# Performance work log

Hardware: AMD Instinct MI355X
Metric: run time of the kernel (lower is better)

Reference implementation:

```python
import jax, jax.numpy as jnp
import numpy as np

N0 = 50000
N1 = 50000
E = 500000
IN_DIM = 128
OUT_DIM = 128
H = 8
DK = OUT_DIM // H  # 16
SQRT_DK = float(np.sqrt(DK))
NUM_TYPES = 2
NUM_REL = 3
# relations: (src_type, dst_type, e_id)
RELATIONS = [(0, 1, 0), (1, 0, 1), (0, 0, 2)]


def setup_inputs() -> dict:
    key = jax.random.key(0)
    ks = jax.random.split(key, 24)
    d = {}
    d["h0"] = jax.random.normal(ks[0], (N0, IN_DIM), dtype=jnp.float32)
    d["h1"] = jax.random.normal(ks[1], (N1, IN_DIM), dtype=jnp.float32)
    d["src0"] = jax.random.randint(ks[2], (E,), 0, N0)
    d["dst0"] = jax.random.randint(ks[3], (E,), 0, N1)
    d["src1"] = jax.random.randint(ks[4], (E,), 0, N1)
    d["dst1"] = jax.random.randint(ks[5], (E,), 0, N0)
    d["src2"] = jax.random.randint(ks[6], (E,), 0, N0)
    d["dst2"] = jax.random.randint(ks[7], (E,), 0, N0)
    w_scale = 1.0 / np.sqrt(IN_DIM)
    # per-node-type stacked linear weights (k, q, v, a), torch Linear convention: y = x @ W.T + b
    d["Wk"] = jax.random.normal(ks[8], (NUM_TYPES, OUT_DIM, IN_DIM), dtype=jnp.float32) * w_scale
    d["bk"] = jnp.zeros((NUM_TYPES, OUT_DIM), dtype=jnp.float32)
    d["Wq"] = jax.random.normal(ks[9], (NUM_TYPES, OUT_DIM, IN_DIM), dtype=jnp.float32) * w_scale
    d["bq"] = jnp.zeros((NUM_TYPES, OUT_DIM), dtype=jnp.float32)
    d["Wv"] = jax.random.normal(ks[10], (NUM_TYPES, OUT_DIM, IN_DIM), dtype=jnp.float32) * w_scale
    d["bv"] = jnp.zeros((NUM_TYPES, OUT_DIM), dtype=jnp.float32)
    d["Wa"] = jax.random.normal(ks[11], (NUM_TYPES, OUT_DIM, OUT_DIM), dtype=jnp.float32) * w_scale
    d["ba"] = jnp.zeros((NUM_TYPES, OUT_DIM), dtype=jnp.float32)
    xavier = float(np.sqrt(6.0 / (DK + DK)))
    d["rel_att"] = jax.random.uniform(ks[12], (NUM_REL, H, DK, DK), dtype=jnp.float32, minval=-xavier, maxval=xavier)
    d["rel_msg"] = jax.random.uniform(ks[13], (NUM_REL, H, DK, DK), dtype=jnp.float32, minval=-xavier, maxval=xavier)
    d["rel_pri"] = jnp.ones((NUM_REL, H), dtype=jnp.float32)
    d["skip"] = jnp.ones((NUM_TYPES,), dtype=jnp.float32)
    return d


def _lin(x, W, b):
    return x @ W.T + b


def reference(h0, h1, src0, dst0, src1, dst1, src2, dst2,
              Wk, bk, Wq, bq, Wv, bv, Wa, ba,
              rel_att, rel_msg, rel_pri, skip):
    h = [h0, h1]
    edges = [(src0, dst0), (src1, dst1), (src2, dst2)]
    # per-type projections, reshaped to (N, H, DK)
    k = [_lin(h[t], Wk[t], bk[t]).reshape(-1, H, DK) for t in range(NUM_TYPES)]
    q = [_lin(h[t], Wq[t], bq[t]).reshape(-1, H, DK) for t in range(NUM_TYPES)]
    v = [_lin(h[t], Wv[t], bv[t]).reshape(-1, H, DK) for t in range(NUM_TYPES)]

    agg = [[] for _ in range(NUM_TYPES)]
    for (s, dt, e), (src, dst) in zip(RELATIONS, edges):
        # relation-specific transforms of source k and v
        kr = jnp.einsum('nhi,hij->nhj', k[s], rel_att[e])
        vr = jnp.einsum('nhi,hij->nhj', v[s], rel_msg[e])
        # per-edge dot-product score (E, H)
        score = (q[dt][dst] * kr[src]).sum(-1) * rel_pri[e] / SQRT_DK
        n_dst = h[dt].shape[0]
        # edge softmax normalized by dst (stable)
        m = jax.ops.segment_max(score, dst, num_segments=n_dst)
        ex = jnp.exp(score - m[dst])
        den = jax.ops.segment_sum(ex, dst, num_segments=n_dst)
        attn = ex / den[dst]  # (E, H)
        # weighted message scatter-sum -> (n_dst, H, DK)
        msg = vr[src] * attn[:, :, None]
        agg[dt].append(jax.ops.segment_sum(msg, dst, num_segments=n_dst))

    new_h = []
    for t in range(NUM_TYPES):
        # cross_reducer='mean' over relations targeting this node type
        tmean = sum(agg[t]) / float(len(agg[t]))
        tflat = tmean.reshape(-1, OUT_DIM)
        trans = _lin(tflat, Wa[t], ba[t])  # dropout = identity (eval)
        alpha = jax.nn.sigmoid(skip[t])
        new_h.append(trans * alpha + h[t] * (1.0 - alpha))
    return tuple(new_h)
```

## Files before the change

### kernel.cpp

```cpp
#include <hip/hip_runtime.h>

typedef __attribute__((ext_vector_type(8))) short bf16x8;
typedef __attribute__((ext_vector_type(4))) float f32x4;

#define NB 196
#define CHK 2048
#define CAPB 4096

__device__ __forceinline__ float bflo(unsigned u) { return __uint_as_float(u << 16); }
__device__ __forceinline__ float bfhi(unsigned u) { return __uint_as_float(u & 0xFFFF0000u); }
__device__ __forceinline__ unsigned f2bf(float f) {
  unsigned u = __float_as_uint(f);
  u = (u + 0x7FFFu + ((u >> 16) & 1u)) >> 16;
  return u;
}

__global__ void cvt2_kernel(const float* __restrict__ a, unsigned short* __restrict__ oa,
                            const float* __restrict__ b, unsigned short* __restrict__ ob,
                            int n8) {
  int i = blockIdx.x * 256 + threadIdx.x;
  if (i >= n8) return;
  const float* in = blockIdx.y ? b : a;
  unsigned short* out = blockIdx.y ? ob : oa;
  const float4* p = (const float4*)(in + (size_t)i * 8);
  float4 x = p[0], y = p[1];
  uint4 v;
  v.x = f2bf(x.x) | (f2bf(x.y) << 16);
  v.y = f2bf(x.z) | (f2bf(x.w) << 16);
  v.z = f2bf(y.x) | (f2bf(y.y) << 16);
  v.w = f2bf(y.z) | (f2bf(y.w) << 16);
  *(uint4*)(out + (size_t)i * 8) = v;
}

__global__ void compose_w_kernel(const float* __restrict__ Wk, const float* __restrict__ bk,
                                 const float* __restrict__ Wv, const float* __restrict__ bv,
                                 const float* __restrict__ rel_att, const float* __restrict__ rel_msg,
                                 const float* __restrict__ rel_pri,
                                 unsigned short* __restrict__ Wkr, float* __restrict__ bkr,
                                 unsigned short* __restrict__ Wvr, float* __restrict__ bvr) {
  int e = blockIdx.x;
  int o = blockIdx.y;
  int z = blockIdx.z;
  int c = threadIdx.x;
  int hd = o >> 4, j = o & 15;
  const int se[3] = {0, 1, 0};
  int s = se[e];
  const float* W = z ? Wv : Wk;
  const float* b = z ? bv : bk;
  const float* R = z ? rel_msg : rel_att;
  float scale = z ? 1.0f : (rel_pri[e * 8 + hd] * 0.25f);
  float acc = 0.0f, bacc = 0.0f;
#pragma unroll
  for (int i = 0; i < 16; ++i) {
    float r = R[((e * 8 + hd) * 16 + i) * 16 + j];
    acc += W[(s * 128 + hd * 16 + i) * 128 + c] * r;
    bacc += b[s * 128 + hd * 16 + i] * r;
  }
  unsigned short* Wo = z ? Wvr : Wkr;
  float* bo = z ? bvr : bkr;
  Wo[((size_t)e * 128 + o) * 128 + c] = (unsigned short)f2bf(acc * scale);
  if (c == 0) bo[e * 128 + o] = bacc * scale;
}

struct ProjFP {
  const float* A[2];
  int M[2];
  int nj[2];
  const unsigned short* W[10];
  const float* b[10];
  unsigned short* out[10];
  int ostr[10];
};

__global__ __launch_bounds__(256) void proj_gemm_fused(ProjFP P) {
  __shared__ short As[128 * 128];
  __shared__ short Bs[128 * 128];
  int type = blockIdx.y;
  const float* __restrict__ A = P.A[type];
  int M = P.M[type];
  int nj = P.nj[type];
  int base = type * 5;
  int row0 = blockIdx.x * 128;
  if (row0 >= M) return;
  int t = threadIdx.x;
  bool full = (row0 + 128 <= M);
#pragma unroll
  for (int it = 0; it < 8; ++it) {
    int o = (it * 256 + t) * 8;
    int row = o >> 7, col = o & 127;
    int gr = row0 + row;
    uint4 av = make_uint4(0, 0, 0, 0);
    if (full || gr < M) {
      float4 x = *(const float4*)(A + (size_t)gr * 128 + col);
      float4 y = *(const float4*)(A + (size_t)gr * 128 + col + 4);
      av.x = f2bf(x.x) | (f2bf(x.y) << 16);
      av.y = f2bf(x.z) | (f2bf(x.w) << 16);
      av.z = f2bf(y.x) | (f2bf(y.y) << 16);
      av.w = f2bf(y.z) | (f2bf(y.w) << 16);
    }
    int sw = o ^ ((row & 7) << 3);
    *(uint4*)(&As[sw]) = av;
  }
  {
    const unsigned short* W0 = P.W[base];
#pragma unroll
    for (int it = 0; it < 8; ++it) {
      int o = (it * 256 + t) * 8;
      int row = o >> 7;
      int sw = o ^ ((row & 7) << 3);
      *(uint4*)(&Bs[sw]) = *(const uint4*)(W0 + o);
    }
  }
  __syncthreads();
  int wid = t >> 6, l = t & 63;
  int wr = wid >> 1, wc = wid & 1;
  int lr = l & 15, kb = l >> 4;
  for (int j = 0;; ++j) {
    f32x4 acc[4][4] = {};
#pragma unroll
    for (int ks = 0; ks < 4; ++ks) {
      bf16x8 af[4], bfr[4];
#pragma unroll
      for (int m = 0; m < 4; ++m) {
        int row = wr * 64 + m * 16 + lr;
        int h = (row * 128 + kb * 8 + ks * 32) ^ ((row & 7) << 3);
        af[m] = *(bf16x8*)(&As[h]);
      }
#pragma unroll
      for (int n = 0; n < 4; ++n) {
        int row = wc * 64 + n * 16 + lr;
        int h = (row * 128 + kb * 8 + ks * 32) ^ ((row & 7) << 3);
        bfr[n] = *(bf16x8*)(&Bs[h]);
      }
#pragma unroll
      for (int m = 0; m < 4; ++m)
#pragma unroll
        for (int n = 0; n < 4; ++n)
          acc[m][n] = __builtin_amdgcn_mfma_f32_16x16x32_bf16(af[m], bfr[n], acc[m][n], 0, 0, 0);
    }
    const float* bias = P.b[base + j];
    unsigned short* out = P.out[base + j];
    int ostr = P.ostr[base + j];
    int rb = row0 + wr * 64 + (l >> 4) * 4;
#pragma unroll
    for (int m = 0; m < 4; ++m)
#pragma unroll
      for (int jr = 0; jr < 4; ++jr) {
        int grow = rb + m * 16 + jr;
        if (grow < M) {
#pragma unroll
          for (int n = 0; n < 4; ++n) {
            int col = wc * 64 + n * 16 + lr;
            out[(size_t)grow * ostr + col] = (unsigned short)f2bf(acc[m][n][jr] + bias[col]);
          }
        }
      }
    if (j + 1 >= nj) break;
    __syncthreads();
    {
      const unsigned short* Wj = P.W[base + j + 1];
#pragma unroll
      for (int it = 0; it < 8; ++it) {
        int o = (it * 256 + t) * 8;
        int row = o >> 7;
        int sw = o ^ ((row & 7) << 3);
        *(uint4*)(&Bs[sw]) = *(const uint4*)(Wj + o);
      }
    }
    __syncthreads();
  }
}

__global__ __launch_bounds__(256) void final_gemm_mfma(
    float* __restrict__ dout, const unsigned short* __restrict__ Tb0,
    const unsigned short* __restrict__ Tb1, const unsigned short* __restrict__ Wab,
    const float* __restrict__ ba, const float* __restrict__ h0, const float* __restrict__ h1,
    const float* __restrict__ skip, int N0, int N1) {
  __shared__ short As[128 * 128];
  __shared__ short Bs[128 * 128];
  int type = blockIdx.y;
  int M = type ? N1 : N0;
  const unsigned short* T = type ? Tb1 : Tb0;
  const unsigned short* W = Wab + (size_t)type * 16384;
  const float* bias = ba + type * 128;
  const float* h = type ? h1 : h0;
  float* O = dout + (type ? (size_t)N0 * 128 : 0);
  int row0 = blockIdx.x * 128;
  if (row0 >= M) return;
  int t = threadIdx.x;
  bool full = (row0 + 128 <= M);
#pragma unroll
  for (int it = 0; it < 8; ++it) {
    int o = (it * 256 + t) * 8;
    int row = o >> 7;
    int gr = row0 + row;
    uint4 av = make_uint4(0, 0, 0, 0);
    if (full || gr < M) av = *(const uint4*)(T + (size_t)gr * 128 + (o & 127));
    int sw = o ^ ((row & 7) << 3);
    *(uint4*)(&As[sw]) = av;
    uint4 wv = *(const uint4*)(W + o);
    *(uint4*)(&Bs[sw]) = wv;
  }
  __syncthreads();
  int wid = t >> 6, l = t & 63;
  int wr = wid >> 1, wc = wid & 1;
  int lr = l & 15, kb = l >> 4;
  f32x4 acc[4][4] = {};
#pragma unroll
  for (int ks = 0; ks < 4; ++ks) {
    bf16x8 af[4], bfr[4];
#pragma unroll
    for (int m = 0; m < 4; ++m) {
      int row = wr * 64 + m * 16 + lr;
      int h2 = (row * 128 + kb * 8 + ks * 32) ^ ((row & 7) << 3);
      af[m] = *(bf16x8*)(&As[h2]);
    }
#pragma unroll
    for (int n = 0; n < 4; ++n) {
      int row = wc * 64 + n * 16 + lr;
      int h2 = (row * 128 + kb * 8 + ks * 32) ^ ((row & 7) << 3);
      bfr[n] = *(bf16x8*)(&Bs[h2]);
    }
#pragma unroll
    for (int m = 0; m < 4; ++m)
#pragma unroll
      for (int n = 0; n < 4; ++n)
        acc[m][n] = __builtin_amdgcn_mfma_f32_16x16x32_bf16(af[m], bfr[n], acc[m][n], 0, 0, 0);
  }
  float alpha = 1.0f / (1.0f + __expf(-skip[type]));
  float beta = 1.0f - alpha;
  int rb = row0 + wr * 64 + (l >> 4) * 4;
#pragma unroll
  for (int m = 0; m < 4; ++m)
#pragma unroll
    for (int jr = 0; jr < 4; ++jr) {
      int grow = rb + m * 16 + jr;
      if (grow < M) {
#pragma unroll
        for (int n = 0; n < 4; ++n) {
          int col = wc * 64 + n * 16 + lr;
          float vout = alpha * (acc[m][n][jr] + bias[col]) + beta * h[(size_t)grow * 128 + col];
          O[(size_t)grow * 128 + col] = vout;
        }
      }
    }
}


__global__ __launch_bounds__(256) void bhist_kernel(const int* __restrict__ d0,
                                                    const int* __restrict__ d1,
                                                    const int* __restrict__ d2,
                                                    int* __restrict__ bh, int E) {
  __shared__ int lh[NB];
  int r = blockIdx.y;
  const int* dst = r == 0 ? d0 : (r == 1 ? d1 : d2);
  int t = threadIdx.x;
  int lo = blockIdx.x * CHK;
  int hi = lo + CHK < E ? lo + CHK : E;
  for (int j = t; j < NB; j += 256) lh[j] = 0;
  __syncthreads();
  for (int i = lo + t; i < hi; i += 256) atomicAdd(&lh[dst[i] >> 8], 1);
  __syncthreads();
  for (int j = t; j < NB; j += 256) {
    int v = lh[j];
    if (v) atomicAdd(&bh[r * NB + j], v);
  }
}

__global__ void bscan_kernel(const int* __restrict__ bh, int* __restrict__ bbase, int E) {
  __shared__ int sdm[256];
  int r = blockIdx.x;
  int t = threadIdx.x;
  int v = (t < NB) ? bh[r * NB + t] : 0;
  sdm[t] = v;
  __syncthreads();
  for (int off = 1; off < 256; off <<= 1) {
    int u = (t >= off) ? sdm[t - off] : 0;
    __syncthreads();
    sdm[t] += u;
    __syncthreads();
  }
  if (t < NB) bbase[r * (NB + 1) + t] = sdm[t] - v;
  if (t == 0) bbase[r * (NB + 1) + NB] = E;
}

__global__ __launch_bounds__(256) void bin_kernel(
    const int* __restrict__ s0, const int* __restrict__ d0, const int* __restrict__ s1,
    const int* __restrict__ d1, const int* __restrict__ s2, const int* __restrict__ d2,
    const int* __restrict__ bbase, int* __restrict__ bcur, unsigned* __restrict__ bo0,
    unsigned* __restrict__ bo1, unsigned* __restrict__ bo2, int E) {
  __shared__ unsigned st[CHK];
  __shared__ int ga[CHK];
  __shared__ int hist[NB];
  __shared__ int scn[256];
  __shared__ int gb[NB];
  int r = blockIdx.y;
  const int* src = r == 0 ? s0 : (r == 1 ? s1 : s2);
  const int* dst = r == 0 ? d0 : (r == 1 ? d1 : d2);
  unsigned* bo = r == 0 ? bo0 : (r == 1 ? bo1 : bo2);
  const int* bb = bbase + r * (NB + 1);
  int t = threadIdx.x;
  int lo = blockIdx.x * CHK;
  int hi = lo + CHK < E ? lo + CHK : E;
  int nloc = hi - lo;
  if (nloc <= 0) return;
  for (int j = t; j < NB; j += 256) hist[j] = 0;
  __syncthreads();
  int myb[CHK / 256], myr[CHK / 256];
  unsigned mye[CHK / 256];
#pragma unroll
  for (int k = 0; k < CHK / 256; ++k) {
    int i = lo + k * 256 + t;
    myb[k] = -1;
    if (i < hi) {
      int d = dst[i];
      int b = d >> 8;
      mye[k] = (unsigned)src[i] | ((unsigned)d << 16);
      myb[k] = b;
      myr[k] = atomicAdd(&hist[b], 1);
    }
  }
  __syncthreads();
  int v = (t < NB) ? hist[t] : 0;
  scn[t] = v;
  __syncthreads();
  for (int off = 1; off < 256; off <<= 1) {
    int u = (t >= off) ? scn[t - off] : 0;
    __syncthreads();
    scn[t] += u;
    __syncthreads();
  }
  int excl = scn[t] - v;
  __syncthreads();
  scn[t] = excl;
  if (t < NB && v > 0) gb[t] = atomicAdd(&bcur[r * NB + t], v);
  __syncthreads();
#pragma unroll
  for (int k = 0; k < CHK / 256; ++k) {
    if (myb[k] >= 0) {
      int slot = scn[myb[k]] + myr[k];
      st[slot] = mye[k];
      ga[slot] = bb[myb[k]] + gb[myb[k]] + myr[k];
    }
  }
  __syncthreads();
  for (int j = t; j < nloc; j += 256) bo[ga[j]] = st[j];
}

__global__ __launch_bounds__(256) void bsort_kernel(
    const unsigned* __restrict__ bo0, const unsigned* __restrict__ bo1,
    const unsigned* __restrict__ bo2, const int* __restrict__ bbase, int* __restrict__ rp0,
    int* __restrict__ rp1, int* __restrict__ rp2, unsigned* __restrict__ sp0,
    unsigned* __restrict__ sp1, unsigned* __restrict__ sp2, int nd0, int nd1, int nd2, int E) {
  __shared__ unsigned ed[CAPB];
  __shared__ unsigned srt[CAPB];
  __shared__ unsigned short rank[CAPB];
  __shared__ int hist[256];
  __shared__ int scn[256];
  int r = blockIdx.y, b = blockIdx.x;
  const unsigned* bo = r == 0 ? bo0 : (r == 1 ? bo1 : bo2);
  int* rp = r == 0 ? rp0 : (r == 1 ? rp1 : rp2);
  unsigned* sp = r == 0 ? sp0 : (r == 1 ? sp1 : sp2);
  int nd = r == 0 ? nd0 : (r == 1 ? nd1 : nd2);
  const int* bb = bbase + r * (NB + 1);
  int base = bb[b], endb = bb[b + 1];
  int cnt = endb - base;
  if (cnt > CAPB) cnt = CAPB;
  int nlo = b << 8;
  int nn = nd - nlo;
  if (nn > 256) nn = 256;
  int t = threadIdx.x;
  hist[t] = 0;
  for (int j = t; j < cnt; j += 256) ed[j] = bo[base + j];
  __syncthreads();
  for (int j = t; j < cnt; j += 256) {
    int node = (ed[j] >> 16) & 255;
    rank[j] = (unsigned short)atomicAdd(&hist[node], 1);
  }
  __syncthreads();
  int v = hist[t];
  scn[t] = v;
  __syncthreads();
  for (int off = 1; off < 256; off <<= 1) {
    int u = (t >= off) ? scn[t - off] : 0;
    __syncthreads();
    scn[t] += u;
    __syncthreads();
  }
  int excl = scn[t] - v;
  __syncthreads();
  scn[t] = excl;
  __syncthreads();
  if (t < nn) rp[nlo + t] = base + excl;
  if (b == 0 && t == 0) rp[nd] = E;
  for (int j = t; j < cnt; j += 256) {
    int node = (ed[j] >> 16) & 255;
    srt[scn[node] + rank[j]] = ed[j];
  }
  __syncthreads();
  for (int j = t; j < cnt; j += 256) sp[base + j] = srt[j];
}

struct ScP {
  const unsigned* sp[3];
  const unsigned* kv[3];
  const unsigned* qb[3];
  unsigned short* eb[3];
  int E;
};

__global__ __launch_bounds__(256) void score_kernel(ScP P) {
  int r = blockIdx.y;
  const unsigned* __restrict__ sp = P.sp[r];
  const unsigned* __restrict__ kv = P.kv[r];
  const unsigned* __restrict__ qb = P.qb[r];
  unsigned short* __restrict__ eb = P.eb[r];
  int t = threadIdx.x;
  int p = blockIdx.x * 32 + (t >> 3);
  if (p >= P.E) return;
  int h = t & 7;
  unsigned pk = sp[p];
  unsigned s = pk & 0xFFFFu;
  unsigned d = pk >> 16;
  const uint4* kr = (const uint4*)((const char*)kv + ((size_t)s << 9) + h * 32);
  const uint4* qr = (const uint4*)((const char*)qb + ((size_t)d << 8) + h * 32);
  uint4 k1 = kr[0], k2 = kr[1];
  uint4 q1 = qr[0], q2 = qr[1];
  float sc = 0.f;
#pragma unroll
  for (int c = 0; c < 4; ++c) {
    unsigned ku = ((const unsigned*)&k1)[c], qu = ((const unsigned*)&q1)[c];
    sc = fmaf(bflo(ku), bflo(qu), sc);
    sc = fmaf(bfhi(ku), bfhi(qu), sc);
  }
#pragma unroll
  for (int c = 0; c < 4; ++c) {
    unsigned ku = ((const unsigned*)&k2)[c], qu = ((const unsigned*)&q2)[c];
    sc = fmaf(bflo(ku), bflo(qu), sc);
    sc = fmaf(bfhi(ku), bfhi(qu), sc);
  }
  eb[(size_t)p * 8 + h] = (unsigned short)f2bf(__expf(sc));
}

struct AgP {
  const unsigned *sp0, *sp1, *sp2;
  const unsigned short *eb0, *eb1, *eb2;
  const unsigned *kv0, *kv1, *kv2;
  const int *rp0, *rp1, *rp2;
  unsigned *Tb0, *Tb1;
  int N0, N1;
};

__device__ __forceinline__ void loadV(const char* __restrict__ kvl,
                                      const unsigned* __restrict__ sp, int p, int lastp,
                                      int half, uint2 vb[4]) {
  int idx = p + (threadIdx.x & 7);
  idx = idx > lastp ? lastp : idx;
  unsigned sv = sp[idx];
#pragma unroll
  for (int g = 0; g < 4; ++g) {
    unsigned plo = __builtin_amdgcn_readlane(sv, g);
    unsigned phi = __builtin_amdgcn_readlane(sv, g + 4);
    unsigned pk = half ? phi : plo;
    vb[g] = *(const uint2*)(kvl + ((size_t)(pk & 0xFFFFu) << 9));
  }
}

__device__ __forceinline__ void computeV(const unsigned short* __restrict__ eb, int p, int end,
                                         int lastp, int half, int h, const uint2 vb[4],
                                         float& a0, float& a1, float& a2, float& a3,
                                         float& den) {
#pragma unroll
  for (int g = 0; g < 4; ++g) {
    int pj = p + (half << 2) + g;
    int pj2 = pj > lastp ? lastp : pj;
    float e = __uint_as_float((unsigned)eb[(size_t)pj2 * 8 + h] << 16);
    e *= (pj < end) ? 1.f : 0.f;
    den += e;
    a0 = fmaf(e, bflo(vb[g].x), a0);
    a1 = fmaf(e, bfhi(vb[g].x), a1);
    a2 = fmaf(e, bflo(vb[g].y), a2);
    a3 = fmaf(e, bfhi(vb[g].y), a3);
  }
}

__device__ __forceinline__ void agg_rel(const unsigned* __restrict__ sp,
                                        const unsigned short* __restrict__ eb,
                                        const unsigned* __restrict__ kv,
                                        const int* __restrict__ rp, int node, int ll, int half,
                                        float& r0, float& r1, float& r2, float& r3) {
  int beg = __builtin_amdgcn_readfirstlane(rp[node]);
  int end = __builtin_amdgcn_readfirstlane(rp[node + 1]);
  if (end <= beg) return;
  int lastp = end - 1;
  int h = ll >> 2;
  const char* kvl = (const char*)kv + 256 + ll * 8;
  float a0 = 0.f, a1 = 0.f, a2 = 0.f, a3 = 0.f, den = 0.f;
  uint2 va[4], vb[4];
  int p = beg;
  loadV(kvl, sp, p, lastp, half, va);
  for (;;) {
    if (p + 8 < end) loadV(kvl, sp, p + 8, lastp, half, vb);
    computeV(eb, p, end, lastp, half, h, va, a0, a1, a2, a3, den);
    p += 8;
    if (p >= end) break;
    if (p + 8 < end) loadV(kvl, sp, p + 8, lastp, half, va);
    computeV(eb, p, end, lastp, half, h, vb, a0, a1, a2, a3, den);
    p += 8;
    if (p >= end) break;
  }
  den += __shfl_xor(den, 32);
  a0 += __shfl_xor(a0, 32);
  a1 += __shfl_xor(a1, 32);
  a2 += __shfl_xor(a2, 32);
  a3 += __shfl_xor(a3, 32);
  float inv = 1.0f / den;
  r0 = fmaf(a0, inv, r0);
  r1 = fmaf(a1, inv, r1);
  r2 = fmaf(a2, inv, r2);
  r3 = fmaf(a3, inv, r3);
}

__global__ __launch_bounds__(256) void agg2_kernel(AgP P) {
  int gw = (blockIdx.x * 256 + threadIdx.x) >> 6;
  int l = threadIdx.x & 63;
  int ll = l & 31, half = l >> 5;
  if (gw < P.N0) {
    float r0 = 0.f, r1 = 0.f, r2 = 0.f, r3 = 0.f;
    agg_rel(P.sp1, P.eb1, P.kv1, P.rp1, gw, ll, half, r0, r1, r2, r3);
    agg_rel(P.sp2, P.eb2, P.kv2, P.rp2, gw, ll, half, r0, r1, r2, r3);
    if (half == 0) {
      uint2 o;
      o.x = f2bf(r0 * 0.5f) | (f2bf(r1 * 0.5f) << 16);
      o.y = f2bf(r2 * 0.5f) | (f2bf(r3 * 0.5f) << 16);
      *(uint2*)(P.Tb0 + (size_t)gw * 64 + 2 * ll) = o;
    }
  } else if (gw < P.N0 + P.N1) {
    int n = gw - P.N0;
    float r0 = 0.f, r1 = 0.f, r2 = 0.f, r3 = 0.f;
    agg_rel(P.sp0, P.eb0, P.kv0, P.rp0, n, ll, half, r0, r1, r2, r3);
    if (half == 0) {
      uint2 o;
      o.x = f2bf(r0) | (f2bf(r1) << 16);
      o.y = f2bf(r2) | (f2bf(r3) << 16);
      *(uint2*)(P.Tb1 + (size_t)n * 64 + 2 * ll) = o;
    }
  }
}

extern "C" void kernel_launch(void* const* d_in, const int* in_sizes, int n_in,
                              void* d_out, int out_size, void* d_ws, size_t ws_size,
                              hipStream_t stream) {
  const float* h0 = (const float*)d_in[0];
  const float* h1 = (const float*)d_in[1];
  const int* srcs[3] = {(const int*)d_in[2], (const int*)d_in[4], (const int*)d_in[6]};
  const int* dsts[3] = {(const int*)d_in[3], (const int*)d_in[5], (const int*)d_in[7]};
  const float* Wk = (const float*)d_in[8];
  const float* bk = (const float*)d_in[9];
  const float* Wq = (const float*)d_in[10];
  const float* bq = (const float*)d_in[11];
  const float* Wv = (const float*)d_in[12];
  const float* bv = (const float*)d_in[13];
  const float* Wa = (const float*)d_in[14];
  const float* ba = (const float*)d_in[15];
  const float* rel_att = (const float*)d_in[16];
  const float* rel_msg = (const float*)d_in[17];
  const float* rel_pri = (const float*)d_in[18];
  const float* skip = (const float*)d_in[19];

  int N0 = in_sizes[0] / 128;
  int N1 = in_sizes[1] / 128;
  int E = in_sizes[2];
  int nsrc[3] = {N0, N1, N0};
  int ndst[3] = {N1, N0, N0};
  int maxN = N0 > N1 ? N0 : N1;

  char* base = (char*)d_ws;
  size_t off = 0;
  auto alloc = [&](size_t bytes) -> void* {
    void* p = base + off;
    off += (bytes + 255) & ~(size_t)255;
    return p;
  };

  unsigned short* qb0 = (unsigned short*)alloc((size_t)N0 * 128 * 2);
  unsigned short* qb1 = (unsigned short*)alloc((size_t)N1 * 128 * 2);
  unsigned short* kvb[3];
  for (int r = 0; r < 3; ++r) kvb[r] = (unsigned short*)alloc((size_t)nsrc[r] * 256 * 2);
  unsigned short* Tb0 = (unsigned short*)alloc((size_t)N0 * 128 * 2);
  unsigned short* Tb1 = (unsigned short*)alloc((size_t)N1 * 128 * 2);
  unsigned short* Wkrb = (unsigned short*)alloc((size_t)3 * 16384 * 2);
  unsigned short* Wvrb = (unsigned short*)alloc((size_t)3 * 16384 * 2);
  unsigned short* Wqb = (unsigned short*)alloc((size_t)2 * 16384 * 2);
  unsigned short* Wab = (unsigned short*)alloc((size_t)2 * 16384 * 2);
  float* bkr = (float*)alloc(3 * 128 * 4);
  float* bvr = (float*)alloc(3 * 128 * 4);
  int* rp[3];
  unsigned* spk[3];
  unsigned short* eb[3];
  unsigned* bo[3];
  for (int r = 0; r < 3; ++r) {
    rp[r] = (int*)alloc((size_t)(ndst[r] + 1) * 4);
    spk[r] = (unsigned*)alloc((size_t)(E + 8) * 4);
    eb[r] = (unsigned short*)alloc((size_t)E * 8 * 2);
    bo[r] = (unsigned*)alloc((size_t)(E + 8) * 4);
  }
  int* bcnt = (int*)alloc((size_t)2 * 3 * NB * 4);
  int* bhist = bcnt;
  int* bcur = bcnt + 3 * NB;
  int* bbase = (int*)alloc((size_t)3 * (NB + 1) * 4);
  (void)ws_size;

  compose_w_kernel<<<dim3(3, 128, 2), 128, 0, stream>>>(Wk, bk, Wv, bv, rel_att, rel_msg,
                                                        rel_pri, Wkrb, bkr, Wvrb, bvr);
  cvt2_kernel<<<dim3(16, 2), 256, 0, stream>>>(Wq, Wqb, Wa, Wab, 4096);

  ProjFP pf;
  pf.A[0] = h0; pf.A[1] = h1;
  pf.M[0] = N0; pf.M[1] = N1;
  pf.nj[0] = 5; pf.nj[1] = 3;
  pf.W[0] = Wqb;            pf.b[0] = bq;        pf.out[0] = qb0;          pf.ostr[0] = 128;
  pf.W[1] = Wkrb;           pf.b[1] = bkr;       pf.out[1] = kvb[0];       pf.ostr[1] = 256;
  pf.W[2] = Wkrb + 32768;   pf.b[2] = bkr + 256; pf.out[2] = kvb[2];       pf.ostr[2] = 256;
  pf.W[3] = Wvrb;           pf.b[3] = bvr;       pf.out[3] = kvb[0] + 128; pf.ostr[3] = 256;
  pf.W[4] = Wvrb + 32768;   pf.b[4] = bvr + 256; pf.out[4] = kvb[2] + 128; pf.ostr[4] = 256;
  pf.W[5] = Wqb + 16384;    pf.b[5] = bq + 128;  pf.out[5] = qb1;          pf.ostr[5] = 128;
  pf.W[6] = Wkrb + 16384;   pf.b[6] = bkr + 128; pf.out[6] = kvb[1];       pf.ostr[6] = 256;
  pf.W[7] = Wvrb + 16384;   pf.b[7] = bvr + 128; pf.out[7] = kvb[1] + 128; pf.ostr[7] = 256;
  pf.W[8] = Wqb; pf.b[8] = bq; pf.out[8] = qb0; pf.ostr[8] = 128;
  pf.W[9] = Wqb; pf.b[9] = bq; pf.out[9] = qb0; pf.ostr[9] = 128;
  proj_gemm_fused<<<dim3((maxN + 127) / 128, 2), 256, 0, stream>>>(pf);

  hipMemsetAsync(bcnt, 0, (size_t)2 * 3 * NB * 4, stream);
  bhist_kernel<<<dim3((E + CHK - 1) / CHK, 3), 256, 0, stream>>>(dsts[0], dsts[1], dsts[2],
                                                                 bhist, E);
  bscan_kernel<<<3, 256, 0, stream>>>(bhist, bbase, E);
  bin_kernel<<<dim3((E + CHK - 1) / CHK, 3), 256, 0, stream>>>(
      srcs[0], dsts[0], srcs[1], dsts[1], srcs[2], dsts[2], bbase, bcur, bo[0], bo[1], bo[2], E);
  bsort_kernel<<<dim3(NB, 3), 256, 0, stream>>>(
      bo[0], bo[1], bo[2], bbase, rp[0], rp[1], rp[2], spk[0], spk[1], spk[2], ndst[0],
      ndst[1], ndst[2], E);

  ScP sp;
  for (int r = 0; r < 3; ++r) {
    sp.sp[r] = spk[r];
    sp.kv[r] = (const unsigned*)kvb[r];
    sp.eb[r] = eb[r];
  }
  sp.qb[0] = (const unsigned*)qb1;
  sp.qb[1] = (const unsigned*)qb0;
  sp.qb[2] = (const unsigned*)qb0;
  sp.E = E;
  score_kernel<<<dim3((E + 31) / 32, 3), 256, 0, stream>>>(sp);

  AgP ap;
  ap.sp0 = spk[0]; ap.sp1 = spk[1]; ap.sp2 = spk[2];
  ap.eb0 = eb[0]; ap.eb1 = eb[1]; ap.eb2 = eb[2];
  ap.kv0 = (const unsigned*)kvb[0]; ap.kv1 = (const unsigned*)kvb[1];
  ap.kv2 = (const unsigned*)kvb[2];
  ap.rp0 = rp[0]; ap.rp1 = rp[1]; ap.rp2 = rp[2];
  ap.Tb0 = (unsigned*)Tb0; ap.Tb1 = (unsigned*)Tb1;
  ap.N0 = N0; ap.N1 = N1;
  int totw = N0 + N1;
  agg2_kernel<<<(totw + 3) / 4, 256, 0, stream>>>(ap);

  final_gemm_mfma<<<dim3((maxN + 127) / 128, 2), 256, 0, stream>>>(
      (float*)d_out, Tb0, Tb1, Wab, ba, h0, h1, skip, N0, N1);
}
```

Measured before the change: 250.0 us.

## Pad per-node edge segments to multiples of eight with head-major score layout

The bucket sort now pads each destination node's edge list to a multiple of 8 with sentinel entries and writes into fixed-stride per-bucket regions, storing separate start/end offsets per node. Scores are stored head-major within each 8-edge group, so the aggregation loop fetches all four exp weights for a lane with one 8-byte load instead of four clamped scalar loads with bounds masking. This removes the tail clamping and masking work in the aggregation inner loop. In exchange, padding adds extra gathered edges and sentinel clamping, and the score grid is oversized with early-exit blocks.

```diff
diff --git a/kernel.cpp b/kernel.cpp
--- a/kernel.cpp
+++ b/kernel.cpp
@@ -6,6 +6,7 @@
 #define NB 196
 #define CHK 2048
 #define CAPB 4096
+#define PSTRIDE 6144
 
 __device__ __forceinline__ float bflo(unsigned u) { return __uint_as_float(u << 16); }
 __device__ __forceinline__ float bfhi(unsigned u) { return __uint_as_float(u & 0xFFFF0000u); }
@@ -349,17 +350,19 @@
 
 __global__ __launch_bounds__(256) void bsort_kernel(
     const unsigned* __restrict__ bo0, const unsigned* __restrict__ bo1,
-    const unsigned* __restrict__ bo2, const int* __restrict__ bbase, int* __restrict__ rp0,
-    int* __restrict__ rp1, int* __restrict__ rp2, unsigned* __restrict__ sp0,
-    unsigned* __restrict__ sp1, unsigned* __restrict__ sp2, int nd0, int nd1, int nd2, int E) {
+    const unsigned* __restrict__ bo2, const int* __restrict__ bbase, int* __restrict__ rs0,
+    int* __restrict__ rs1, int* __restrict__ rs2, int* __restrict__ re0, int* __restrict__ re1,
+    int* __restrict__ re2, unsigned* __restrict__ sp0, unsigned* __restrict__ sp1,
+    unsigned* __restrict__ sp2, int* __restrict__ bused, int nd0, int nd1, int nd2) {
   __shared__ unsigned ed[CAPB];
-  __shared__ unsigned srt[CAPB];
+  __shared__ unsigned srt[PSTRIDE];
   __shared__ unsigned short rank[CAPB];
   __shared__ int hist[256];
   __shared__ int scn[256];
   int r = blockIdx.y, b = blockIdx.x;
   const unsigned* bo = r == 0 ? bo0 : (r == 1 ? bo1 : bo2);
-  int* rp = r == 0 ? rp0 : (r == 1 ? rp1 : rp2);
+  int* rs = r == 0 ? rs0 : (r == 1 ? rs1 : rs2);
+  int* re = r == 0 ? re0 : (r == 1 ? re1 : re2);
   unsigned* sp = r == 0 ? sp0 : (r == 1 ? sp1 : sp2);
   int nd = r == 0 ? nd0 : (r == 1 ? nd1 : nd2);
   const int* bb = bbase + r * (NB + 1);
@@ -369,6 +372,7 @@
   int nlo = b << 8;
   int nn = nd - nlo;
   if (nn > 256) nn = 256;
+  if (nn < 0) nn = 0;
   int t = threadIdx.x;
   hist[t] = 0;
   for (int j = t; j < cnt; j += 256) ed[j] = bo[base + j];
@@ -378,8 +382,9 @@
     rank[j] = (unsigned short)atomicAdd(&hist[node], 1);
   }
   __syncthreads();
-  int v = hist[t];
-  scn[t] = v;
+  int rawh = hist[t];
+  int pd = (rawh + 7) & ~7;
+  scn[t] = pd;
   __syncthreads();
   for (int off = 1; off < 256; off <<= 1) {
     int u = (t >= off) ? scn[t - off] : 0;
@@ -387,18 +392,26 @@
     scn[t] += u;
     __syncthreads();
   }
-  int excl = scn[t] - v;
-  __syncthreads();
-  scn[t] = excl;
-  __syncthreads();
-  if (t < nn) rp[nlo + t] = base + excl;
-  if (b == 0 && t == 0) rp[nd] = E;
+  int pexcl = scn[t] - pd;
+  int ptot = scn[255];
+  __syncthreads();
+  hist[t] = pexcl;
+  __syncthreads();
+  if (t < nn) {
+    rs[nlo + t] = b * PSTRIDE + pexcl;
+    re[nlo + t] = b * PSTRIDE + pexcl + pd;
+  }
+  int ptot32 = (ptot + 31) & ~31;
+  for (int j = t; j < ptot32; j += 256) srt[j] = 0xFFFFFFFFu;
+  __syncthreads();
   for (int j = t; j < cnt; j += 256) {
     int node = (ed[j] >> 16) & 255;
-    srt[scn[node] + rank[j]] = ed[j];
-  }
-  __syncthreads();
-  for (int j = t; j < cnt; j += 256) sp[base + j] = srt[j];
+    srt[hist[node] + rank[j]] = ed[j];
+  }
+  __syncthreads();
+  unsigned* spb = sp + (size_t)b * PSTRIDE;
+  for (int j = t; j < ptot32; j += 256) spb[j] = srt[j];
+  if (t == 0) bused[r * NB + b] = ptot32;
 }
 
 struct ScP {
@@ -406,24 +419,34 @@
   const unsigned* kv[3];
   const unsigned* qb[3];
   unsigned short* eb[3];
-  int E;
+  const int* bused;
+  int ns[3];
+  int ndv[3];
 };
 
 __global__ __launch_bounds__(256) void score_kernel(ScP P) {
   int r = blockIdx.y;
+  int bx = blockIdx.x;
+  int bucket = bx / (PSTRIDE / 32);
+  int off = (bx % (PSTRIDE / 32)) * 32;
+  int used = P.bused[r * NB + bucket];
+  if (off >= used) return;
   const unsigned* __restrict__ sp = P.sp[r];
   const unsigned* __restrict__ kv = P.kv[r];
   const unsigned* __restrict__ qb = P.qb[r];
   unsigned short* __restrict__ eb = P.eb[r];
+  unsigned smax = (unsigned)P.ns[r] - 1;
+  unsigned dmax = (unsigned)P.ndv[r] - 1;
   int t = threadIdx.x;
-  int p = blockIdx.x * 32 + (t >> 3);
-  if (p >= P.E) return;
+  int p = bucket * PSTRIDE + off + (t >> 3);
   int h = t & 7;
   unsigned pk = sp[p];
   unsigned s = pk & 0xFFFFu;
   unsigned d = pk >> 16;
-  const uint4* kr = (const uint4*)((const char*)kv + ((size_t)s << 9) + h * 32);
-  const uint4* qr = (const uint4*)((const char*)qb + ((size_t)d << 8) + h * 32);
+  unsigned sc2 = s > smax ? smax : s;
+  unsigned dc = d > dmax ? dmax : d;
+  const uint4* kr = (const uint4*)((const char*)kv + ((size_t)sc2 << 9) + h * 32);
+  const uint4* qr = (const uint4*)((const char*)qb + ((size_t)dc << 8) + h * 32);
   uint4 k1 = kr[0], k2 = kr[1];
   uint4 q1 = qr[0], q2 = qr[1];
   float sc = 0.f;
@@ -439,43 +462,44 @@
     sc = fmaf(bflo(ku), bflo(qu), sc);
     sc = fmaf(bfhi(ku), bfhi(qu), sc);
   }
-  eb[(size_t)p * 8 + h] = (unsigned short)f2bf(__expf(sc));
+  float e = (s == 0xFFFFu) ? 0.f : __expf(sc);
+  eb[(size_t)(p & ~7) * 8 + h * 8 + (p & 7)] = (unsigned short)f2bf(e);
 }
 
 struct AgP {
   const unsigned *sp0, *sp1, *sp2;
   const unsigned short *eb0, *eb1, *eb2;
   const unsigned *kv0, *kv1, *kv2;
-  const int *rp0, *rp1, *rp2;
+  const int *rs0, *rs1, *rs2;
+  const int *re0, *re1, *re2;
   unsigned *Tb0, *Tb1;
+  int ns0, ns1, ns2;
   int N0, N1;
 };
 
 __device__ __forceinline__ void loadV(const char* __restrict__ kvl,
-                                      const unsigned* __restrict__ sp, int p, int lastp,
-                                      int half, uint2 vb[4]) {
-  int idx = p + (threadIdx.x & 7);
-  idx = idx > lastp ? lastp : idx;
-  unsigned sv = sp[idx];
+                                      const unsigned* __restrict__ sp,
+                                      const unsigned short* __restrict__ eb, int p,
+                                      unsigned smax, int half, int h, uint2 vb[4], uint2& ev) {
+  unsigned sv = sp[p + (threadIdx.x & 7)];
+  ev = *(const uint2*)(eb + (size_t)p * 8 + h * 8 + half * 4);
 #pragma unroll
   for (int g = 0; g < 4; ++g) {
     unsigned plo = __builtin_amdgcn_readlane(sv, g);
     unsigned phi = __builtin_amdgcn_readlane(sv, g + 4);
     unsigned pk = half ? phi : plo;
-    vb[g] = *(const uint2*)(kvl + ((size_t)(pk & 0xFFFFu) << 9));
-  }
-}
-
-__device__ __forceinline__ void computeV(const unsigned short* __restrict__ eb, int p, int end,
-                                         int lastp, int half, int h, const uint2 vb[4],
-                                         float& a0, float& a1, float& a2, float& a3,
-                                         float& den) {
+    unsigned s = pk & 0xFFFFu;
+    s = s > smax ? smax : s;
+    vb[g] = *(const uint2*)(kvl + ((size_t)s << 9));
+  }
+}
+
+__device__ __forceinline__ void computeV(const uint2 vb[4], uint2 ev, float& a0, float& a1,
+                                         float& a2, float& a3, float& den) {
+  float eg[4] = {bflo(ev.x), bfhi(ev.x), bflo(ev.y), bfhi(ev.y)};
 #pragma unroll
   for (int g = 0; g < 4; ++g) {
-    int pj = p + (half << 2) + g;
-    int pj2 = pj > lastp ? lastp : pj;
-    float e = __uint_as_float((unsigned)eb[(size_t)pj2 * 8 + h] << 16);
-    e *= (pj < end) ? 1.f : 0.f;
+    float e = eg[g];
     den += e;
     a0 = fmaf(e, bflo(vb[g].x), a0);
     a1 = fmaf(e, bfhi(vb[g].x), a1);
@@ -487,25 +511,26 @@
 __device__ __forceinline__ void agg_rel(const unsigned* __restrict__ sp,
                                         const unsigned short* __restrict__ eb,
                                         const unsigned* __restrict__ kv,
-                                        const int* __restrict__ rp, int node, int ll, int half,
+                                        const int* __restrict__ rs, const int* __restrict__ re,
+                                        int node, int ll, int half, unsigned smax,
                                         float& r0, float& r1, float& r2, float& r3) {
-  int beg = __builtin_amdgcn_readfirstlane(rp[node]);
-  int end = __builtin_amdgcn_readfirstlane(rp[node + 1]);
+  int beg = __builtin_amdgcn_readfirstlane(rs[node]);
+  int end = __builtin_amdgcn_readfirstlane(re[node]);
   if (end <= beg) return;
-  int lastp = end - 1;
   int h = ll >> 2;
   const char* kvl = (const char*)kv + 256 + ll * 8;
   float a0 = 0.f, a1 = 0.f, a2 = 0.f, a3 = 0.f, den = 0.f;
   uint2 va[4], vb[4];
+  uint2 ea, ebv;
   int p = beg;
-  loadV(kvl, sp, p, lastp, half, va);
+  loadV(kvl, sp, eb, p, smax, half, h, va, ea);
   for (;;) {
-    if (p + 8 < end) loadV(kvl, sp, p + 8, lastp, half, vb);
-    computeV(eb, p, end, lastp, half, h, va, a0, a1, a2, a3, den);
+    if (p + 8 < end) loadV(kvl, sp, eb, p + 8, smax, half, h, vb, ebv);
+    computeV(va, ea, a0, a1, a2, a3, den);
     p += 8;
     if (p >= end) break;
-    if (p + 8 < end) loadV(kvl, sp, p + 8, lastp, half, va);
-    computeV(eb, p, end, lastp, half, h, vb, a0, a1, a2, a3, den);
+    if (p + 8 < end) loadV(kvl, sp, eb, p + 8, smax, half, h, va, ea);
+    computeV(vb, ebv, a0, a1, a2, a3, den);
     p += 8;
     if (p >= end) break;
   }
@@ -527,8 +552,8 @@
   int ll = l & 31, half = l >> 5;
   if (gw < P.N0) {
     float r0 = 0.f, r1 = 0.f, r2 = 0.f, r3 = 0.f;
-    agg_rel(P.sp1, P.eb1, P.kv1, P.rp1, gw, ll, half, r0, r1, r2, r3);
-    agg_rel(P.sp2, P.eb2, P.kv2, P.rp2, gw, ll, half, r0, r1, r2, r3);
+    agg_rel(P.sp1, P.eb1, P.kv1, P.rs1, P.re1, gw, ll, half, (unsigned)P.ns1 - 1, r0, r1, r2, r3);
+    agg_rel(P.sp2, P.eb2, P.kv2, P.rs2, P.re2, gw, ll, half, (unsigned)P.ns2 - 1, r0, r1, r2, r3);
     if (half == 0) {
       uint2 o;
       o.x = f2bf(r0 * 0.5f) | (f2bf(r1 * 0.5f) << 16);
@@ -538,7 +563,7 @@
   } else if (gw < P.N0 + P.N1) {
     int n = gw - P.N0;
     float r0 = 0.f, r1 = 0.f, r2 = 0.f, r3 = 0.f;
-    agg_rel(P.sp0, P.eb0, P.kv0, P.rp0, n, ll, half, r0, r1, r2, r3);
+    agg_rel(P.sp0, P.eb0, P.kv0, P.rs0, P.re0, n, ll, half, (unsigned)P.ns0 - 1, r0, r1, r2, r3);
     if (half == 0) {
       uint2 o;
       o.x = f2bf(r0) | (f2bf(r1) << 16);
@@ -595,20 +620,23 @@
   unsigned short* Wab = (unsigned short*)alloc((size_t)2 * 16384 * 2);
   float* bkr = (float*)alloc(3 * 128 * 4);
   float* bvr = (float*)alloc(3 * 128 * 4);
-  int* rp[3];
+  int* rp_s[3];
+  int* rp_e[3];
   unsigned* spk[3];
   unsigned short* eb[3];
   unsigned* bo[3];
   for (int r = 0; r < 3; ++r) {
-    rp[r] = (int*)alloc((size_t)(ndst[r] + 1) * 4);
-    spk[r] = (unsigned*)alloc((size_t)(E + 8) * 4);
-    eb[r] = (unsigned short*)alloc((size_t)E * 8 * 2);
+    rp_s[r] = (int*)alloc((size_t)ndst[r] * 4);
+    rp_e[r] = (int*)alloc((size_t)ndst[r] * 4);
+    spk[r] = (unsigned*)alloc((size_t)NB * PSTRIDE * 4);
+    eb[r] = (unsigned short*)alloc((size_t)NB * PSTRIDE * 8 * 2);
     bo[r] = (unsigned*)alloc((size_t)(E + 8) * 4);
   }
   int* bcnt = (int*)alloc((size_t)2 * 3 * NB * 4);
   int* bhist = bcnt;
   int* bcur = bcnt + 3 * NB;
   int* bbase = (int*)alloc((size_t)3 * (NB + 1) * 4);
+  int* bused = (int*)alloc((size_t)3 * NB * 4);
   (void)ws_size;
 
   compose_w_kernel<<<dim3(3, 128, 2), 128, 0, stream>>>(Wk, bk, Wv, bv, rel_att, rel_msg,
@@ -638,27 +666,31 @@
   bin_kernel<<<dim3((E + CHK - 1) / CHK, 3), 256, 0, stream>>>(
       srcs[0], dsts[0], srcs[1], dsts[1], srcs[2], dsts[2], bbase, bcur, bo[0], bo[1], bo[2], E);
   bsort_kernel<<<dim3(NB, 3), 256, 0, stream>>>(
-      bo[0], bo[1], bo[2], bbase, rp[0], rp[1], rp[2], spk[0], spk[1], spk[2], ndst[0],
-      ndst[1], ndst[2], E);
+      bo[0], bo[1], bo[2], bbase, rp_s[0], rp_s[1], rp_s[2], rp_e[0], rp_e[1], rp_e[2],
+      spk[0], spk[1], spk[2], bused, ndst[0], ndst[1], ndst[2]);
 
   ScP sp;
   for (int r = 0; r < 3; ++r) {
     sp.sp[r] = spk[r];
     sp.kv[r] = (const unsigned*)kvb[r];
     sp.eb[r] = eb[r];
-  }
+    sp.ns[r] = nsrc[r];
+    sp.ndv[r] = ndst[r];
+  }
+  sp.bused = bused;
   sp.qb[0] = (const unsigned*)qb1;
   sp.qb[1] = (const unsigned*)qb0;
   sp.qb[2] = (const unsigned*)qb0;
-  sp.E = E;
-  score_kernel<<<dim3((E + 31) / 32, 3), 256, 0, stream>>>(sp);
+  score_kernel<<<dim3(NB * (PSTRIDE / 32), 3), 256, 0, stream>>>(sp);
 
   AgP ap;
   ap.sp0 = spk[0]; ap.sp1 = spk[1]; ap.sp2 = spk[2];
   ap.eb0 = eb[0]; ap.eb1 = eb[1]; ap.eb2 = eb[2];
   ap.kv0 = (const unsigned*)kvb[0]; ap.kv1 = (const unsigned*)kvb[1];
   ap.kv2 = (const unsigned*)kvb[2];
-  ap.rp0 = rp[0]; ap.rp1 = rp[1]; ap.rp2 = rp[2];
+  ap.rs0 = rp_s[0]; ap.rs1 = rp_s[1]; ap.rs2 = rp_s[2];
+  ap.re0 = rp_e[0]; ap.re1 = rp_e[1]; ap.re2 = rp_e[2];
+  ap.ns0 = nsrc[0]; ap.ns1 = nsrc[1]; ap.ns2 = nsrc[2];
   ap.Tb0 = (unsigned*)Tb0; ap.Tb1 = (unsigned*)Tb1;
   ap.N0 = N0; ap.N1 = N1;
   int totw = N0 + N1;
```

Measured after the change: 263.4 us. +5.4%, slower.
